# Optimization experiments

Hardware: AMD Instinct MI355X
Metric: run time of the kernel (lower is better)

The kernel has to match this reference:

```python
import jax, jax.numpy as jnp
import numpy as np

N_NODES = 50000
N_EDGES = 600000
HIDDEN = 128
NUM_CLASSES = 5
NUM_NODE_FEATURES = 3
NUM_GRAPHS = 128


def setup_inputs() -> dict:
    key = jax.random.key(0)
    ks = jax.random.split(key, 12)
    x = jax.random.normal(ks[0], (N_NODES, NUM_NODE_FEATURES), dtype=jnp.float32)
    edge_index = jax.random.randint(ks[1], (2, N_EDGES), 0, N_NODES, dtype=jnp.int64)
    batch = jnp.sort(jax.random.randint(ks[2], (N_NODES,), 0, NUM_GRAPHS, dtype=jnp.int64))
    def glorot(k, fan_in, fan_out):
        s = jnp.sqrt(6.0 / (fan_in + fan_out)).astype(jnp.float32)
        return jax.random.uniform(k, (fan_in, fan_out), jnp.float32, -s, s)
    return {
        "x": x,
        "edge_index": edge_index,
        "batch": batch,
        "W1": glorot(ks[3], NUM_NODE_FEATURES, HIDDEN), "b1": jnp.zeros((HIDDEN,), jnp.float32),
        "W2": glorot(ks[4], HIDDEN, HIDDEN), "b2": jnp.zeros((HIDDEN,), jnp.float32),
        "W3": glorot(ks[5], HIDDEN, HIDDEN), "b3": jnp.zeros((HIDDEN,), jnp.float32),
        "Wl": glorot(ks[6], HIDDEN, NUM_CLASSES), "bl": jnp.zeros((NUM_CLASSES,), jnp.float32),
    }


def _gcn_norm(edge_index, n_nodes):
    # Add self loops, compute symmetric normalization D^-1/2 (A+I) D^-1/2.
    loops = jnp.arange(n_nodes, dtype=edge_index.dtype)
    src = jnp.concatenate([edge_index[0], loops])
    dst = jnp.concatenate([edge_index[1], loops])
    ones = jnp.ones(src.shape[0], dtype=jnp.float32)
    deg = jax.ops.segment_sum(ones, dst, num_segments=n_nodes)
    dis = jnp.where(deg > 0, jax.lax.rsqrt(jnp.maximum(deg, 1.0)), 0.0)
    norm = dis[src] * dis[dst]  # [E + N]
    return src, dst, norm


def _gcn_conv(h, W, b, src, dst, norm, n_nodes):
    h = h @ W                              # [N, out]
    msg = h[src] * norm[:, None]           # gather + scale: [E+N, out]
    out = jax.ops.segment_sum(msg, dst, num_segments=n_nodes)  # scatter-add
    return out + b


def reference(x, edge_index, batch, W1, b1, W2, b2, W3, b3, Wl, bl):
    n = x.shape[0]
    src, dst, norm = _gcn_norm(edge_index, n)
    h = jax.nn.relu(_gcn_conv(x, W1, b1, src, dst, norm, n))
    h = jax.nn.relu(_gcn_conv(h, W2, b2, src, dst, norm, n))
    h = jax.nn.relu(_gcn_conv(h, W3, b3, src, dst, norm, n))
    # global_mean_pool over graphs
    sums = jax.ops.segment_sum(h, batch, num_segments=NUM_GRAPHS)
    cnts = jax.ops.segment_sum(jnp.ones((n,), jnp.float32), batch, num_segments=NUM_GRAPHS)
    fingerprint = sums / jnp.maximum(cnts, 1.0)[:, None]  # [G, HIDDEN]
    # dropout is identity in eval mode
    return fingerprint @ Wl + bl  # [G, NUM_CLASSES]
```

## Files before the change

### kernel.cpp

```cpp
#include <hip/hip_runtime.h>

#define N_NODES   50000
#define N_EDGES   600000
#define HID       128
#define N_GRAPHS  128
#define N_CLASSES 5
#define POOL_CHUNK 32
#define PREP_BLK  ((N_NODES + 255) / 256)
#define RSTRIDE   40

__global__ void k_fill2(const int* __restrict__ src, const int* __restrict__ dst,
                        int* __restrict__ cursor, int* __restrict__ col, int E) {
    int i = blockIdx.x * blockDim.x + threadIdx.x;
    if (i < E) {
        int d = dst[i];
        int pos = atomicAdd(&cursor[d], 1);
        if (pos < RSTRIDE) col[d * RSTRIDE + pos] = src[i];
    }
}

__global__ void k_prep(const int* __restrict__ cursor, const float* __restrict__ x,
                       float* __restrict__ dis, float4* __restrict__ xs,
                       const int* __restrict__ batch, int* __restrict__ gcnt, int n) {
    if (blockIdx.x == gridDim.x - 1) {
        __shared__ int s[N_GRAPHS + 1];
        int t = threadIdx.x;
        if (t <= N_GRAPHS) {
            int lo = 0, hi = n;
            while (lo < hi) {
                int mid = (lo + hi) >> 1;
                if (batch[mid] < t) lo = mid + 1; else hi = mid;
            }
            s[t] = lo;
        }
        __syncthreads();
        if (t < N_GRAPHS) gcnt[t] = s[t + 1] - s[t];
        return;
    }
    int i = blockIdx.x * 256 + threadIdx.x;
    if (i < n) {
        float dd = 1.0f / sqrtf((float)cursor[i] + 1.0f);
        dis[i] = dd;
        float4 o;
        o.x = dd * x[i * 3 + 0];
        o.y = dd * x[i * 3 + 1];
        o.z = dd * x[i * 3 + 2];
        o.w = 0.f;
        xs[i] = o;
    }
}

__global__ __launch_bounds__(256) void k_agg3l1(const float4* __restrict__ xs,
                                                const float* __restrict__ dis,
                                                const int* __restrict__ deg,
                                                const int* __restrict__ col,
                                                const float* __restrict__ W1,
                                                const float* __restrict__ b1,
                                                float* __restrict__ out) {
    __shared__ float Wls[3 * HID];
    __shared__ float bls[HID];
    int t = threadIdx.x;
    for (int i = t; i < 3 * HID; i += 256) Wls[i] = W1[i];
    for (int i = t; i < HID; i += 256) bls[i] = b1[i];
    __syncthreads();

    int g = t >> 2;
    int f = t & 3;
    int d = blockIdx.x * 64 + g;
    if (d >= N_NODES) return;
    const float* xsf = (const float*)xs;
    int j0 = d * RSTRIDE;
    int j1 = j0 + min(deg[d], RSTRIDE);
    float a0 = xsf[(size_t)d * 4 + f];
    float a1 = 0.f, a2 = 0.f, a3 = 0.f;
    int j = j0;
    for (; j + 3 < j1; j += 4) {
        int s0 = col[j], s1 = col[j + 1], s2 = col[j + 2], s3 = col[j + 3];
        a0 += xsf[(size_t)s0 * 4 + f];
        a1 += xsf[(size_t)s1 * 4 + f];
        a2 += xsf[(size_t)s2 * 4 + f];
        a3 += xsf[(size_t)s3 * 4 + f];
    }
    for (; j < j1; ++j)
        a0 += xsf[(size_t)col[j] * 4 + f];
    float val = dis[d] * ((a0 + a1) + (a2 + a3));

    int base = (t & 63) & ~3;
    float av0 = __shfl(val, base + 0);
    float av1 = __shfl(val, base + 1);
    float av2 = __shfl(val, base + 2);

    const float* w0 = &Wls[0 * HID];
    const float* w1 = &Wls[1 * HID];
    const float* w2 = &Wls[2 * HID];
    int c0 = f * 32;
#pragma unroll
    for (int c4 = 0; c4 < 8; ++c4) {
        int c = c0 + c4 * 4;
        float4 o;
        o.x = fmaxf(fmaf(av2, w2[c + 0], fmaf(av1, w1[c + 0], fmaf(av0, w0[c + 0], bls[c + 0]))), 0.f);
        o.y = fmaxf(fmaf(av2, w2[c + 1], fmaf(av1, w1[c + 1], fmaf(av0, w0[c + 1], bls[c + 1]))), 0.f);
        o.z = fmaxf(fmaf(av2, w2[c + 2], fmaf(av1, w1[c + 2], fmaf(av0, w0[c + 2], bls[c + 2]))), 0.f);
        o.w = fmaxf(fmaf(av2, w2[c + 3], fmaf(av1, w1[c + 3], fmaf(av0, w0[c + 3], bls[c + 3]))), 0.f);
        *(float4*)&out[(size_t)d * HID + c] = o;
    }
}

__global__ __launch_bounds__(512, 2) void k_gemm128(const float* __restrict__ h,
                                                    const float* __restrict__ W,
                                                    const float* __restrict__ dis,
                                                    float* __restrict__ out, int n) {
    __shared__ float Ws[HID * HID];
    __shared__ float Hs[2][128 * 8];
    int t  = threadIdx.x;
    int tc = t & 31;
    int tr = t >> 5;
    int row0 = blockIdx.x * 128 + tr * 8;

    {
        const float4* wg = (const float4*)W;
        float4* wsv = (float4*)Ws;
#pragma unroll
        for (int i = 0; i < 8; ++i)
            wsv[i * 512 + t] = wg[i * 512 + t];
    }

    int srow = blockIdx.x * 128 + (t >> 1);
    if (srow >= n) srow = n - 1;
    const float* hsrc = h + (size_t)srow * HID + (t & 1) * 4;
    int sidx = (t >> 1) * 8 + (t & 1) * 4;
    if (t < 256)
        *(float4*)&Hs[0][sidx] = *(const float4*)hsrc;

    float acc[8][4];
#pragma unroll
    for (int r = 0; r < 8; ++r)
#pragma unroll
        for (int c = 0; c < 4; ++c) acc[r][c] = 0.f;

    __syncthreads();

    int buf = 0;
    for (int k0 = 0; k0 < HID; k0 += 8) {
        float4 pf;
        bool do_pf = (k0 + 8 < HID) && (t < 256);
        if (do_pf) pf = *(const float4*)(hsrc + k0 + 8);

        float4 hv4[8];
#pragma unroll
        for (int r = 0; r < 8; ++r)
            hv4[r] = *(const float4*)&Hs[buf][(tr * 8 + r) * 8];
#pragma unroll
        for (int kk = 0; kk < 4; ++kk) {
            float4 wv = *(const float4*)&Ws[(k0 + kk) * HID + tc * 4];
#pragma unroll
            for (int r = 0; r < 8; ++r) {
                float hv = kk == 0 ? hv4[r].x : kk == 1 ? hv4[r].y : kk == 2 ? hv4[r].z : hv4[r].w;
                acc[r][0] = fmaf(hv, wv.x, acc[r][0]);
                acc[r][1] = fmaf(hv, wv.y, acc[r][1]);
                acc[r][2] = fmaf(hv, wv.z, acc[r][2]);
                acc[r][3] = fmaf(hv, wv.w, acc[r][3]);
            }
        }
#pragma unroll
        for (int r = 0; r < 8; ++r)
            hv4[r] = *(const float4*)&Hs[buf][(tr * 8 + r) * 8 + 4];
#pragma unroll
        for (int kk = 0; kk < 4; ++kk) {
            float4 wv = *(const float4*)&Ws[(k0 + 4 + kk) * HID + tc * 4];
#pragma unroll
            for (int r = 0; r < 8; ++r) {
                float hv = kk == 0 ? hv4[r].x : kk == 1 ? hv4[r].y : kk == 2 ? hv4[r].z : hv4[r].w;
                acc[r][0] = fmaf(hv, wv.x, acc[r][0]);
                acc[r][1] = fmaf(hv, wv.y, acc[r][1]);
                acc[r][2] = fmaf(hv, wv.z, acc[r][2]);
                acc[r][3] = fmaf(hv, wv.w, acc[r][3]);
            }
        }

        if (do_pf) *(float4*)&Hs[buf ^ 1][sidx] = pf;
        __syncthreads();
        buf ^= 1;
    }

#pragma unroll
    for (int r = 0; r < 8; ++r) {
        int row = row0 + r;
        if (row < n) {
            float dd = dis[row];
            float4 o;
            o.x = dd * acc[r][0]; o.y = dd * acc[r][1];
            o.z = dd * acc[r][2]; o.w = dd * acc[r][3];
            *(float4*)&out[(size_t)row * HID + tc * 4] = o;
        }
    }
}

__global__ __launch_bounds__(256) void k_agg(const float* __restrict__ t,
                                             const float* __restrict__ dis,
                                             const int* __restrict__ deg,
                                             const int* __restrict__ col,
                                             const float* __restrict__ bias,
                                             float* __restrict__ out) {
    int lane = threadIdx.x & 31;
    int wid  = threadIdx.x >> 5;
    int d = blockIdx.x * 8 + wid;
    if (d >= N_NODES) return;
    const float4* t4 = (const float4*)t;
    float4 bv = ((const float4*)bias)[lane];
    float dd = dis[d];
    int j0 = d * RSTRIDE;
    int j1 = j0 + min(deg[d], RSTRIDE);
    float4 self = t4[(size_t)d * 32 + lane];
    float x0 = self.x, y0 = self.y, z0 = self.z, w0 = self.w;
    float x1 = 0.f, y1 = 0.f, z1 = 0.f, w1 = 0.f;
    float x2 = 0.f, y2 = 0.f, z2 = 0.f, w2 = 0.f;
    float x3 = 0.f, y3 = 0.f, z3 = 0.f, w3 = 0.f;
    int j = j0;
    for (; j + 3 < j1; j += 4) {
        int s0 = col[j], s1 = col[j + 1], s2 = col[j + 2], s3 = col[j + 3];
        float4 v0 = t4[(size_t)s0 * 32 + lane];
        float4 v1 = t4[(size_t)s1 * 32 + lane];
        float4 v2 = t4[(size_t)s2 * 32 + lane];
        float4 v3 = t4[(size_t)s3 * 32 + lane];
        x0 += v0.x; y0 += v0.y; z0 += v0.z; w0 += v0.w;
        x1 += v1.x; y1 += v1.y; z1 += v1.z; w1 += v1.w;
        x2 += v2.x; y2 += v2.y; z2 += v2.z; w2 += v2.w;
        x3 += v3.x; y3 += v3.y; z3 += v3.z; w3 += v3.w;
    }
    for (; j < j1; ++j) {
        int s = col[j];
        float4 v = t4[(size_t)s * 32 + lane];
        x0 += v.x; y0 += v.y; z0 += v.z; w0 += v.w;
    }
    float sx = (x0 + x1) + (x2 + x3);
    float sy = (y0 + y1) + (y2 + y3);
    float sz = (z0 + z1) + (z2 + z3);
    float sw = (w0 + w1) + (w2 + w3);
    float4 o;
    o.x = fmaxf(fmaf(dd, sx, bv.x), 0.f);
    o.y = fmaxf(fmaf(dd, sy, bv.y), 0.f);
    o.z = fmaxf(fmaf(dd, sz, bv.z), 0.f);
    o.w = fmaxf(fmaf(dd, sw, bv.w), 0.f);
    ((float4*)out)[(size_t)d * 32 + lane] = o;
}

__global__ void k_psum(const float* __restrict__ h, const int* __restrict__ batch,
                       float* __restrict__ fpsum, int n) {
    int i0 = blockIdx.x * POOL_CHUNK;
    int f = threadIdx.x;
    int end = min(i0 + POOL_CHUNK, n);
    int cur = batch[i0];
    float acc = 0.f;
    for (int i = i0; i < end; ++i) {
        int g = batch[i];
        if (g != cur) {
            atomicAdd(&fpsum[cur * HID + f], acc);
            acc = 0.f;
            cur = g;
        }
        acc += h[(size_t)i * HID + f];
    }
    atomicAdd(&fpsum[cur * HID + f], acc);
}

__global__ void k_final(const float* __restrict__ fpsum, const int* __restrict__ gcnt,
                        const float* __restrict__ Wl, const float* __restrict__ bl,
                        float* __restrict__ out) {
    int idx = blockIdx.x * blockDim.x + threadIdx.x;
    if (idx >= N_GRAPHS * N_CLASSES) return;
    int g = idx / N_CLASSES, c = idx % N_CLASSES;
    float inv = 1.0f / (float)max(gcnt[g], 1);
    float acc = bl[c];
    for (int f = 0; f < HID; ++f)
        acc = fmaf(fpsum[g * HID + f] * inv, Wl[f * N_CLASSES + c], acc);
    out[idx] = acc;
}

extern "C" void kernel_launch(void* const* d_in, const int* in_sizes, int n_in,
                              void* d_out, int out_size, void* d_ws, size_t ws_size,
                              hipStream_t stream) {
    const float* x     = (const float*)d_in[0];
    const int*   ei    = (const int*)d_in[1];
    const int*   batch = (const int*)d_in[2];
    const float* W1 = (const float*)d_in[3];
    const float* b1 = (const float*)d_in[4];
    const float* W2 = (const float*)d_in[5];
    const float* b2 = (const float*)d_in[6];
    const float* W3 = (const float*)d_in[7];
    const float* b3 = (const float*)d_in[8];
    const float* Wl = (const float*)d_in[9];
    const float* bl = (const float*)d_in[10];
    float* out = (float*)d_out;

    const int N = N_NODES, E = N_EDGES;
    const int* srcp = ei;
    const int* dstp = ei + E;

    char* ws = (char*)d_ws;
    size_t off = 0;
    auto alloc = [&](size_t bytes) -> void* {
        void* p = ws + off;
        off += (bytes + 255) & ~(size_t)255;
        return p;
    };
    int*   cursor = (int*)alloc((size_t)N * 4);
    float* fpsum  = (float*)alloc((size_t)N_GRAPHS * HID * 4);
    size_t zero_bytes = off;
    int*   gcnt  = (int*)alloc((size_t)N_GRAPHS * 4);
    float* dis   = (float*)alloc((size_t)N * 4);
    int*   col   = (int*)alloc((size_t)N * RSTRIDE * 4);
    float* bufA  = (float*)alloc((size_t)N * HID * 4);
    float* bufB  = (float*)alloc((size_t)N * HID * 4);
    float4* xs   = (float4*)alloc((size_t)N * 16);

    hipMemsetAsync(d_ws, 0, zero_bytes, stream);

    const int tpb = 256;
    k_fill2<<<(E + tpb - 1) / tpb, tpb, 0, stream>>>(srcp, dstp, cursor, col, E);
    k_prep<<<PREP_BLK + 1, 256, 0, stream>>>(cursor, x, dis, xs, batch, gcnt, N);

    k_agg3l1<<<(N + 63) / 64, 256, 0, stream>>>(xs, dis, cursor, col, W1, b1, bufB);
    k_gemm128<<<(N + 127) / 128, 512, 0, stream>>>(bufB, W2, dis, bufA, N);
    k_agg<<<(N + 7) / 8, 256, 0, stream>>>(bufA, dis, cursor, col, b2, bufB);
    k_gemm128<<<(N + 127) / 128, 512, 0, stream>>>(bufB, W3, dis, bufA, N);
    k_agg<<<(N + 7) / 8, 256, 0, stream>>>(bufA, dis, cursor, col, b3, bufB);
    k_psum<<<(N + POOL_CHUNK - 1) / POOL_CHUNK, HID, 0, stream>>>(bufB, batch, fpsum, N);
    k_final<<<(N_GRAPHS * N_CLASSES + tpb - 1) / tpb, tpb, 0, stream>>>(fpsum, gcnt, Wl, bl, out);
}
```

Measured before the change: 320.5 us.

## Use 16-bit neighbor indices and fuse final aggregation with mean pooling

Stores CSR column indices as unsigned short, since the node count fits in 16 bits. This halves index memory traffic and lets four indices load as one vector. Also fuses the last GCN aggregation with the graph pooling partial sums: a block-level shared-memory reduction plus atomics replaces writing the full hidden buffer and reading it back in a separate pooling kernel. This relies on the node count staying below 65536 and adds atomic contention on the pooled sums.

```diff
diff --git a/kernel.cpp b/kernel.cpp
--- a/kernel.cpp
+++ b/kernel.cpp
@@ -5,17 +5,16 @@
 #define HID       128
 #define N_GRAPHS  128
 #define N_CLASSES 5
-#define POOL_CHUNK 32
 #define PREP_BLK  ((N_NODES + 255) / 256)
 #define RSTRIDE   40
 
 __global__ void k_fill2(const int* __restrict__ src, const int* __restrict__ dst,
-                        int* __restrict__ cursor, int* __restrict__ col, int E) {
+                        int* __restrict__ cursor, unsigned short* __restrict__ col, int E) {
     int i = blockIdx.x * blockDim.x + threadIdx.x;
     if (i < E) {
         int d = dst[i];
         int pos = atomicAdd(&cursor[d], 1);
-        if (pos < RSTRIDE) col[d * RSTRIDE + pos] = src[i];
+        if (pos < RSTRIDE) col[d * RSTRIDE + pos] = (unsigned short)src[i];
     }
 }
 
@@ -53,7 +52,7 @@
 __global__ __launch_bounds__(256) void k_agg3l1(const float4* __restrict__ xs,
                                                 const float* __restrict__ dis,
                                                 const int* __restrict__ deg,
-                                                const int* __restrict__ col,
+                                                const unsigned short* __restrict__ col,
                                                 const float* __restrict__ W1,
                                                 const float* __restrict__ b1,
                                                 float* __restrict__ out) {
@@ -199,7 +198,7 @@
 __global__ __launch_bounds__(256) void k_agg(const float* __restrict__ t,
                                              const float* __restrict__ dis,
                                              const int* __restrict__ deg,
-                                             const int* __restrict__ col,
+                                             const unsigned short* __restrict__ col,
                                              const float* __restrict__ bias,
                                              float* __restrict__ out) {
     int lane = threadIdx.x & 31;
@@ -218,11 +217,11 @@
     float x3 = 0.f, y3 = 0.f, z3 = 0.f, w3 = 0.f;
     int j = j0;
     for (; j + 3 < j1; j += 4) {
-        int s0 = col[j], s1 = col[j + 1], s2 = col[j + 2], s3 = col[j + 3];
-        float4 v0 = t4[(size_t)s0 * 32 + lane];
-        float4 v1 = t4[(size_t)s1 * 32 + lane];
-        float4 v2 = t4[(size_t)s2 * 32 + lane];
-        float4 v3 = t4[(size_t)s3 * 32 + lane];
+        ushort4 sv = *(const ushort4*)&col[j];
+        float4 v0 = t4[(size_t)sv.x * 32 + lane];
+        float4 v1 = t4[(size_t)sv.y * 32 + lane];
+        float4 v2 = t4[(size_t)sv.z * 32 + lane];
+        float4 v3 = t4[(size_t)sv.w * 32 + lane];
         x0 += v0.x; y0 += v0.y; z0 += v0.z; w0 += v0.w;
         x1 += v1.x; y1 += v1.y; z1 += v1.z; w1 += v1.w;
         x2 += v2.x; y2 += v2.y; z2 += v2.z; w2 += v2.w;
@@ -245,23 +244,82 @@
     ((float4*)out)[(size_t)d * 32 + lane] = o;
 }
 
-__global__ void k_psum(const float* __restrict__ h, const int* __restrict__ batch,
-                       float* __restrict__ fpsum, int n) {
-    int i0 = blockIdx.x * POOL_CHUNK;
+__global__ __launch_bounds__(256) void k_aggpool(const float* __restrict__ t,
+                                                 const float* __restrict__ dis,
+                                                 const int* __restrict__ deg,
+                                                 const unsigned short* __restrict__ col,
+                                                 const float* __restrict__ bias,
+                                                 const int* __restrict__ batch,
+                                                 float* __restrict__ fpsum) {
+    __shared__ float sh[8][HID];
+    __shared__ int bg[8];
+    int lane = threadIdx.x & 31;
+    int wid  = threadIdx.x >> 5;
+    int d = blockIdx.x * 8 + wid;
+    bool valid = (d < N_NODES);
+    if (lane == 0) bg[wid] = valid ? batch[d] : -1;
+    __syncthreads();
+    int g0 = bg[0];
+
+    float4 o = make_float4(0.f, 0.f, 0.f, 0.f);
+    if (valid) {
+        const float4* t4 = (const float4*)t;
+        float4 bv = ((const float4*)bias)[lane];
+        float dd = dis[d];
+        int j0 = d * RSTRIDE;
+        int j1 = j0 + min(deg[d], RSTRIDE);
+        float4 self = t4[(size_t)d * 32 + lane];
+        float x0 = self.x, y0 = self.y, z0 = self.z, w0 = self.w;
+        float x1 = 0.f, y1 = 0.f, z1 = 0.f, w1 = 0.f;
+        float x2 = 0.f, y2 = 0.f, z2 = 0.f, w2 = 0.f;
+        float x3 = 0.f, y3 = 0.f, z3 = 0.f, w3 = 0.f;
+        int j = j0;
+        for (; j + 3 < j1; j += 4) {
+            ushort4 sv = *(const ushort4*)&col[j];
+            float4 v0 = t4[(size_t)sv.x * 32 + lane];
+            float4 v1 = t4[(size_t)sv.y * 32 + lane];
+            float4 v2 = t4[(size_t)sv.z * 32 + lane];
+            float4 v3 = t4[(size_t)sv.w * 32 + lane];
+            x0 += v0.x; y0 += v0.y; z0 += v0.z; w0 += v0.w;
+            x1 += v1.x; y1 += v1.y; z1 += v1.z; w1 += v1.w;
+            x2 += v2.x; y2 += v2.y; z2 += v2.z; w2 += v2.w;
+            x3 += v3.x; y3 += v3.y; z3 += v3.z; w3 += v3.w;
+        }
+        for (; j < j1; ++j) {
+            int s = col[j];
+            float4 v = t4[(size_t)s * 32 + lane];
+            x0 += v.x; y0 += v.y; z0 += v.z; w0 += v.w;
+        }
+        float sx = (x0 + x1) + (x2 + x3);
+        float sy = (y0 + y1) + (y2 + y3);
+        float sz = (z0 + z1) + (z2 + z3);
+        float sw = (w0 + w1) + (w2 + w3);
+        o.x = fmaxf(fmaf(dd, sx, bv.x), 0.f);
+        o.y = fmaxf(fmaf(dd, sy, bv.y), 0.f);
+        o.z = fmaxf(fmaf(dd, sz, bv.z), 0.f);
+        o.w = fmaxf(fmaf(dd, sw, bv.w), 0.f);
+    }
+
+    if (valid) {
+        if (bg[wid] == g0) {
+            *(float4*)&sh[wid][lane * 4] = o;
+        } else {
+            int g = bg[wid];
+            atomicAdd(&fpsum[g * HID + lane * 4 + 0], o.x);
+            atomicAdd(&fpsum[g * HID + lane * 4 + 1], o.y);
+            atomicAdd(&fpsum[g * HID + lane * 4 + 2], o.z);
+            atomicAdd(&fpsum[g * HID + lane * 4 + 3], o.w);
+        }
+    }
+    __syncthreads();
     int f = threadIdx.x;
-    int end = min(i0 + POOL_CHUNK, n);
-    int cur = batch[i0];
-    float acc = 0.f;
-    for (int i = i0; i < end; ++i) {
-        int g = batch[i];
-        if (g != cur) {
-            atomicAdd(&fpsum[cur * HID + f], acc);
-            acc = 0.f;
-            cur = g;
-        }
-        acc += h[(size_t)i * HID + f];
-    }
-    atomicAdd(&fpsum[cur * HID + f], acc);
+    if (f < HID) {
+        float s = 0.f;
+#pragma unroll
+        for (int w = 0; w < 8; ++w)
+            if (bg[w] == g0) s += sh[w][f];
+        atomicAdd(&fpsum[g0 * HID + f], s);
+    }
 }
 
 __global__ void k_final(const float* __restrict__ fpsum, const int* __restrict__ gcnt,
@@ -309,7 +367,7 @@
     size_t zero_bytes = off;
     int*   gcnt  = (int*)alloc((size_t)N_GRAPHS * 4);
     float* dis   = (float*)alloc((size_t)N * 4);
-    int*   col   = (int*)alloc((size_t)N * RSTRIDE * 4);
+    unsigned short* col = (unsigned short*)alloc((size_t)N * RSTRIDE * 2);
     float* bufA  = (float*)alloc((size_t)N * HID * 4);
     float* bufB  = (float*)alloc((size_t)N * HID * 4);
     float4* xs   = (float4*)alloc((size_t)N * 16);
@@ -324,7 +382,6 @@
     k_gemm128<<<(N + 127) / 128, 512, 0, stream>>>(bufB, W2, dis, bufA, N);
     k_agg<<<(N + 7) / 8, 256, 0, stream>>>(bufA, dis, cursor, col, b2, bufB);
     k_gemm128<<<(N + 127) / 128, 512, 0, stream>>>(bufB, W3, dis, bufA, N);
-    k_agg<<<(N + 7) / 8, 256, 0, stream>>>(bufA, dis, cursor, col, b3, bufB);
-    k_psum<<<(N + POOL_CHUNK - 1) / POOL_CHUNK, HID, 0, stream>>>(bufB, batch, fpsum, N);
+    k_aggpool<<<(N + 7) / 8, 256, 0, stream>>>(bufA, dis, cursor, col, b3, batch, fpsum);
     k_final<<<(N_GRAPHS * N_CLASSES + tpb - 1) / tpb, tpb, 0, stream>>>(fpsum, gcnt, Wl, bl, out);
 }
```

Measured after the change: 302.9 us (median of 2 runs). 5.5% less time.
